# Kernel optimization log

Hardware: AMD Instinct MI355X
Metric: run time of the kernel (lower is better)

The kernel has to match this reference:

```python
import jax, jax.numpy as jnp
import numpy as np

M = 4
L_LIST = [5, 7, 9, 11]
C = 256
GC = C // M  # group channels = 64
BN_EPS = 1e-5


def setup_inputs() -> dict:
    key = jax.random.key(0)
    ks = jax.random.split(key, 12)
    B, H, W = 4, 128, 128
    x = jax.random.normal(ks[0], (B, C, H, W), dtype=jnp.float32)
    # per-group 1x1 conv weights (no bias), stacked since same shape
    qw = jax.random.normal(ks[1], (M, GC, GC), dtype=jnp.float32) * 0.05
    kw = jax.random.normal(ks[2], (M, GC, GC), dtype=jnp.float32) * 0.05
    r_q = jax.random.normal(ks[3], (1, C, 1, 1), dtype=jnp.float32)
    rk0 = jax.random.normal(ks[4], (1, GC, 2 * L_LIST[0] - 1, 1, 1), dtype=jnp.float32)
    rk1 = jax.random.normal(ks[5], (1, GC, 2 * L_LIST[1] - 1, 1, 1), dtype=jnp.float32)
    rk2 = jax.random.normal(ks[6], (1, GC, 2 * L_LIST[2] - 1, 1, 1), dtype=jnp.float32)
    rk3 = jax.random.normal(ks[7], (1, GC, 2 * L_LIST[3] - 1, 1, 1), dtype=jnp.float32)
    fusion_w = jax.random.normal(ks[8], (C, C), dtype=jnp.float32) * 0.05
    bn_gamma = jnp.ones((C,), dtype=jnp.float32)
    bn_beta = jnp.zeros((C,), dtype=jnp.float32)
    return {"x": x, "qw": qw, "kw": kw, "r_q": r_q, "rk0": rk0, "rk1": rk1,
            "rk2": rk2, "rk3": rk3, "fusion_w": fusion_w,
            "bn_gamma": bn_gamma, "bn_beta": bn_beta}


def _axial(k, L):
    """Gather the cross-shaped (axial) neighborhood of size 2L-1 per pixel.

    Matches F.unfold(k, (L,L), padding=pad) followed by slicing the center
    column (vertical neighbors) and center row minus the center element
    (horizontal neighbors), in the original ordering:
      [k_h (L vertical), k_w_pre (pad left), k_w_post (L-pad-1 right)].
    Returns [B, gc, 2L-1, H, W] with zero padding at borders.
    """
    pad = (L - 1) // 2
    B, gc, H, W = k.shape
    kv = jnp.pad(k, ((0, 0), (0, 0), (pad, pad), (0, 0)))
    kh = jnp.pad(k, ((0, 0), (0, 0), (0, 0), (pad, pad)))
    parts = [kv[:, :, r:r + H, :] for r in range(L)]            # vertical offsets -pad..pad
    parts += [kh[:, :, :, r:r + W] for r in range(pad)]          # horizontal -pad..-1
    parts += [kh[:, :, :, r:r + W] for r in range(pad + 1, L)]   # horizontal +1..+pad
    return jnp.stack(parts, axis=2)


def reference(x, qw, kw, r_q, rk0, rk1, rk2, rk3, fusion_w, bn_gamma, bn_beta):
    rks = [rk0, rk1, rk2, rk3]
    B, Cc, H, W = x.shape
    qx = r_q + x
    outs = []
    for i, L in enumerate(L_LIST):
        xg = x[:, i * GC:(i + 1) * GC]
        qg = qx[:, i * GC:(i + 1) * GC]
        q = jnp.einsum('oc,bchw->bohw', qw[i], qg)   # 1x1 conv, no bias
        k = jnp.einsum('oc,bchw->bohw', kw[i], xg)
        ka = _axial(k, L) + rks[i]                   # [B, gc, 2L-1, H, W]
        # energy over channels then summed over the 2L-1 axial positions
        e = jnp.einsum('bchw,bcrhw->bhw', q, ka)
        outs.append(jnp.broadcast_to(e[:, None], (B, GC, H, W)))
    att = jnp.concatenate(outs, axis=1)              # [B, C, H, W]
    att = jnp.einsum('oc,bchw->bohw', fusion_w, att)
    # BatchNorm2d in training mode: batch statistics over (B, H, W)
    mean = att.mean(axis=(0, 2, 3))
    var = att.var(axis=(0, 2, 3))
    att = (att - mean[:, None, None]) * jax.lax.rsqrt(var[:, None, None] + BN_EPS)
    att = att * bn_gamma[:, None, None] + bn_beta[:, None, None]
    att = jax.nn.sigmoid(jax.nn.relu(att))
    return x * att
```

## Files before the change

kernel.cpp:

```cpp
#include <hip/hip_runtime.h>

#define Bb 4
#define Cc 256
#define GC_ 64
#define Hh 128
#define Wd 128
#define HWn 16384
#define NPIX 65536
#define EPS 1e-5f

#define T_OFF   0
#define E_OFF   16777216
#define ST_OFF  (E_OFF + NPIX*4)
#define A_OFF   (ST_OFF + 16)
#define CV_OFF  (A_OFF + 16384)
#define FW_OFF  (CV_OFF + 256)

typedef __attribute__((ext_vector_type(8))) short short8v;
typedef __attribute__((ext_vector_type(4))) float f32x4;
typedef unsigned short u16;

__device__ inline u16 f2bf(float f) {
    union { float f; unsigned u; } v; v.f = f;
    unsigned r = v.u + 0x7fff + ((v.u >> 16) & 1);
    return (u16)(r >> 16);
}
__device__ inline float bf2f(u16 u) {
    union { unsigned u; float f; } v; v.u = ((unsigned)u) << 16;
    return v.f;
}

__global__ __launch_bounds__(256) void k0_precompute(
    const float* __restrict__ qw, const float* __restrict__ kw,
    const float* __restrict__ rk0, const float* __restrict__ rk1,
    const float* __restrict__ rk2, const float* __restrict__ rk3,
    const float* __restrict__ fusion_w,
    u16* __restrict__ Abf, float* __restrict__ cvec, float* __restrict__ fwred,
    float* __restrict__ stats)
{
    const int tid = threadIdx.x;
    if (blockIdx.x == 4) {
        if (tid < 16) stats[tid] = 0.f;
        for (int i = 0; i < 4; ++i) {
            float s = 0.f;
            const float* fp = fusion_w + tid*256 + i*64;
            #pragma unroll 8
            for (int c = 0; c < 64; ++c) s += fp[c];
            fwred[tid*4 + i] = s;
        }
        return;
    }
    const int g = blockIdx.x;
    __shared__ float qwL[4096];
    __shared__ float kwL[4096];
    __shared__ float rks[64];
    for (int i = tid; i < 4096; i += 256) {
        qwL[i] = qw[g*4096 + i];
        kwL[i] = kw[g*4096 + i];
    }
    __syncthreads();
    if (tid < 64) {
        const float* rkp = (g==0)?rk0:(g==1)?rk1:(g==2)?rk2:rk3;
        const int R = 4*g + 9;
        float s = 0.f;
        for (int r = 0; r < R; ++r) s += rkp[tid*R + r];
        rks[tid] = s;
    }
    __syncthreads();
    for (int idx = tid; idx < 4096; idx += 256) {
        const int ct = idx >> 10, kh = (idx >> 9) & 1;
        const int lane = (idx >> 3) & 63, j = idx & 7;
        const int c = ct*16 + (lane & 15);
        const int d = kh*32 + (lane >> 4)*8 + j;
        float s = 0.f;
        #pragma unroll
        for (int o = 0; o < 64; ++o) s += qwL[o*64 + c] * kwL[o*64 + d];
        Abf[g*4096 + idx] = f2bf(s);
    }
    if (tid < 64) {
        float s = 0.f;
        #pragma unroll
        for (int o = 0; o < 64; ++o) s += qwL[o*64 + tid] * rks[o];
        cvec[g*64 + tid] = s;
    }
}

__global__ __launch_bounds__(256) void k1_mfma(
    const float* __restrict__ x, const u16* __restrict__ Abf,
    u16* __restrict__ t, u16* __restrict__ xbf)
{
    __shared__ u16 xt[64*132];
    const int tid = threadIdx.x;
    const int wv = tid >> 6, lane = tid & 63;
    const int chunk = blockIdx.x & 127;
    const int g = (blockIdx.x >> 7) & 3;
    const int b = blockIdx.x >> 9;
    const int l15 = lane & 15, lg = lane >> 4;
    const int px0 = chunk*128;

    const u16* Ab = Abf + g*4096;
    short8v afr[4][2];
    #pragma unroll
    for (int ct = 0; ct < 4; ++ct)
      #pragma unroll
      for (int kh = 0; kh < 2; ++kh)
        afr[ct][kh] = *(const short8v*)(Ab + ((ct*2 + kh)*64 + lane)*8);

    const float* xg = x   + (size_t)(b*Cc + g*GC_)*HWn;
    u16* tg        = t    + (size_t)(b*Cc + g*GC_)*HWn;
    u16* xbg       = xbf  + (size_t)(b*Cc + g*GC_)*HWn;

    #pragma unroll
    for (int i = 0; i < 8; ++i) {
        const int idx = tid + i*256;
        const int ch = idx >> 5, q = (idx & 31) << 2;
        const float4 v = *(const float4*)(xg + (size_t)ch*HWn + px0 + q);
        u16 o4[4] __attribute__((aligned(8))) = {f2bf(v.x), f2bf(v.y), f2bf(v.z), f2bf(v.w)};
        *(uint2*)(xt + ch*132 + q) = *(const uint2*)o4;
        *(uint2*)(xbg + (size_t)ch*HWn + px0 + q) = *(const uint2*)o4;
    }
    __syncthreads();

    const int pw = wv*32;
    #pragma unroll
    for (int nt = 0; nt < 2; ++nt) {
        const int pt = pw + nt*16 + l15;
        short8v bfr[2];
        #pragma unroll
        for (int kh = 0; kh < 2; ++kh)
          #pragma unroll
          for (int j = 0; j < 8; ++j)
            bfr[kh][j] = (short)xt[(kh*32 + lg*8 + j)*132 + pt];
        #pragma unroll
        for (int ct = 0; ct < 4; ++ct) {
            f32x4 acc = {0.f, 0.f, 0.f, 0.f};
            acc = __builtin_amdgcn_mfma_f32_16x16x32_bf16(bfr[0], afr[ct][0], acc, 0, 0, 0);
            acc = __builtin_amdgcn_mfma_f32_16x16x32_bf16(bfr[1], afr[ct][1], acc, 0, 0, 0);
            u16 ov[4] __attribute__((aligned(8)));
            #pragma unroll
            for (int r = 0; r < 4; ++r) ov[r] = f2bf(acc[r]);
            *(uint2*)(tg + (size_t)(ct*16 + l15)*HWn + px0 + pw + nt*16 + lg*4) = *(const uint2*)ov;
        }
    }
}

#define TROW 132
__global__ __launch_bounds__(256) void k2_cross(
    const u16* __restrict__ t, u16* __restrict__ S)
{
    __shared__ u16 timg[42*TROW];
    __shared__ u16 simg[32*TROW];
    const int tid = threadIdx.x;
    const int bid = blockIdx.x;
    const int wk = (bid & 7)*512 + (bid >> 3);
    const int tile = wk & 3;
    const int bc = wk >> 2;
    const int g = (bc & 255) >> 6;
    const int p = g + 2;
    const int h0 = tile * 32;
    const int nrows = 32 + 2*p;
    const u16* tp = t + (size_t)bc*HWn;

    for (int idx = tid; idx < nrows*32; idx += 256) {
        const int r = idx >> 5, w4 = (idx & 31) << 2;
        const int hh = h0 - p + r;
        uint2 v = make_uint2(0u, 0u);
        if (hh >= 0 && hh < 128) v = *(const uint2*)(tp + (hh<<7) + w4);
        *(uint2*)(timg + r*TROW + w4) = v;
    }
    __syncthreads();

    {
        const int w = tid & 127;
        const int half = tid >> 7;
        const int rbase = half * 16;
        float run = 0.f;
        for (int j = 0; j <= 2*p; ++j) run += bf2f(timg[(rbase + j)*TROW + w]);
        #pragma unroll
        for (int i = 0; i < 16; ++i) {
            simg[(rbase + i)*TROW + w] = f2bf(run);
            if (i != 15)
                run += bf2f(timg[(rbase + i + 1 + 2*p)*TROW + w])
                     - bf2f(timg[(rbase + i)*TROW + w]);
        }
    }
    __syncthreads();

    {
        const int r8 = tid >> 3;
        const int seg = tid & 7;
        const int w0 = seg * 16;
        const u16* trow = timg + (r8 + p)*TROW;
        float run = 0.f;
        const int lo = max(w0 - p, 0), hi = min(w0 + p, 127);
        for (int ww = lo; ww <= hi; ++ww) run += bf2f(trow[ww]);
        u16 ov[16] __attribute__((aligned(16)));
        #pragma unroll
        for (int j = 0; j < 16; ++j) {
            const int w = w0 + j;
            const float sv = bf2f(simg[r8*TROW + w]);
            ov[j] = f2bf(run + sv - bf2f(trow[w]));
            run += (w + 1 + p < 128 ? bf2f(trow[w + 1 + p]) : 0.f)
                 - (w - p     >= 0  ? bf2f(trow[w - p])     : 0.f);
        }
        uint4* dst = (uint4*)(S + (size_t)bc*HWn + ((h0 + r8) << 7) + w0);
        dst[0] = ((const uint4*)ov)[0];
        dst[1] = ((const uint4*)ov)[1];
    }
}

__global__ __launch_bounds__(256) void k3_e(
    const u16* __restrict__ xbf, const u16* __restrict__ S,
    const float* __restrict__ r_q, const float* __restrict__ cvec,
    float* __restrict__ ebuf)
{
    const int tid = threadIdx.x;
    const int chunk = blockIdx.x & 63;
    const int g = (blockIdx.x >> 6) & 3;
    const int b = blockIdx.x >> 8;
    __shared__ float rqL[64], cvL[64];
    if (tid < 64) { rqL[tid] = r_q[g*64 + tid]; cvL[tid] = cvec[g*64 + tid]; }
    __syncthreads();
    const int p = chunk*256 + tid;
    const u16* xp = xbf + (size_t)(b*Cc + g*GC_)*HWn + p;
    const u16* Sp = S   + (size_t)(b*Cc + g*GC_)*HWn + p;
    float acc = 0.f;
    #pragma unroll 16
    for (int c = 0; c < 64; ++c)
        acc += (bf2f(xp[c*HWn]) + rqL[c]) * (bf2f(Sp[c*HWn]) + cvL[c]);
    ebuf[(b*4 + g)*HWn + p] = acc;
}

__global__ __launch_bounds__(256) void k3b_stats(
    const float* __restrict__ ebuf, float* __restrict__ stats)
{
    __shared__ float red[4*14];
    const int tid = threadIdx.x;
    const int q = blockIdx.x*256 + tid;
    const int b = q >> 14, p = q & (HWn - 1);
    const float* eb = ebuf + (size_t)b*4*HWn;
    const float e0 = eb[0*HWn + p], e1 = eb[1*HWn + p], e2 = eb[2*HWn + p], e3 = eb[3*HWn + p];
    float v[14];
    v[0]=e0; v[1]=e1; v[2]=e2; v[3]=e3;
    v[4]=e0*e0; v[5]=e0*e1; v[6]=e0*e2; v[7]=e0*e3;
    v[8]=e1*e1; v[9]=e1*e2; v[10]=e1*e3;
    v[11]=e2*e2; v[12]=e2*e3; v[13]=e3*e3;
    #pragma unroll
    for (int kk = 0; kk < 14; ++kk) {
        float s = v[kk];
        for (int off = 32; off > 0; off >>= 1) s += __shfl_down(s, off, 64);
        v[kk] = s;
    }
    const int lane = tid & 63, wv = tid >> 6;
    if (lane == 0) {
        #pragma unroll
        for (int kk = 0; kk < 14; ++kk) red[wv*14 + kk] = v[kk];
    }
    __syncthreads();
    if (tid < 14) atomicAdd(&stats[tid], red[tid] + red[14+tid] + red[28+tid] + red[42+tid]);
}

__global__ __launch_bounds__(256) void k5_out(
    const u16* __restrict__ xbf, const float* __restrict__ ebuf,
    const float* __restrict__ fwred, const float* __restrict__ stats,
    const float* __restrict__ gamma, const float* __restrict__ beta,
    float* __restrict__ out)
{
    const int tid = threadIdx.x;
    const int chunk = blockIdx.x & 15;
    const int oct = (blockIdx.x >> 4) & 31;
    const int b = blockIdx.x >> 9;
    __shared__ float alL[8], beL[8];
    __shared__ float4 fwL[8];
    if (tid < 8) {
        const int o = oct*8 + tid;
        const float invN = 1.f / (float)NPIX;
        const float me0 = stats[0]*invN, me1 = stats[1]*invN, me2 = stats[2]*invN, me3 = stats[3]*invN;
        const float m00 = stats[4]*invN,  m01 = stats[5]*invN,  m02 = stats[6]*invN,  m03 = stats[7]*invN;
        const float m11 = stats[8]*invN,  m12 = stats[9]*invN,  m13 = stats[10]*invN;
        const float m22 = stats[11]*invN, m23 = stats[12]*invN, m33 = stats[13]*invN;
        const float4 fw = ((const float4*)fwred)[o];
        const float Ef = fw.x*me0 + fw.y*me1 + fw.z*me2 + fw.w*me3;
        const float E2 = fw.x*fw.x*m00 + fw.y*fw.y*m11 + fw.z*fw.z*m22 + fw.w*fw.w*m33
                       + 2.f*(fw.x*fw.y*m01 + fw.x*fw.z*m02 + fw.x*fw.w*m03
                            + fw.y*fw.z*m12 + fw.y*fw.w*m13 + fw.z*fw.w*m23);
        const float a = gamma[o] * rsqrtf(E2 - Ef*Ef + EPS);
        alL[tid] = a;
        beL[tid] = beta[o] - Ef*a;
        fwL[tid] = fw;
    }
    __syncthreads();

    const int p0 = chunk*1024 + tid*4;
    const float* eb = ebuf + (size_t)b*4*HWn;
    const float4 E0 = *(const float4*)(eb + 0*HWn + p0);
    const float4 E1 = *(const float4*)(eb + 1*HWn + p0);
    const float4 E2v = *(const float4*)(eb + 2*HWn + p0);
    const float4 E3 = *(const float4*)(eb + 3*HWn + p0);

    #pragma unroll
    for (int c = 0; c < 8; ++c) {
        const int o = oct*8 + c;
        const float4 fw = fwL[c];
        const float al = alL[c], be = beL[c];
        float f[4];
        f[0] = fw.x*E0.x + fw.y*E1.x + fw.z*E2v.x + fw.w*E3.x;
        f[1] = fw.x*E0.y + fw.y*E1.y + fw.z*E2v.y + fw.w*E3.y;
        f[2] = fw.x*E0.z + fw.y*E1.z + fw.z*E2v.z + fw.w*E3.z;
        f[3] = fw.x*E0.w + fw.y*E1.w + fw.z*E2v.w + fw.w*E3.w;
        const size_t base = (size_t)(b*Cc + o)*HWn + p0;
        const uint2 xu = *(const uint2*)(xbf + base);
        float xa[4];
        xa[0] = bf2f((u16)(xu.x & 0xffff)); xa[1] = bf2f((u16)(xu.x >> 16));
        xa[2] = bf2f((u16)(xu.y & 0xffff)); xa[3] = bf2f((u16)(xu.y >> 16));
        float4 r; float* rp = &r.x;
        #pragma unroll
        for (int j = 0; j < 4; ++j) {
            float z = al*f[j] + be;
            z = fmaxf(z, 0.f);
            rp[j] = xa[j] / (1.f + __expf(-z));
        }
        *(float4*)(out + base) = r;
    }
}

extern "C" void kernel_launch(void* const* d_in, const int* in_sizes, int n_in,
                              void* d_out, int out_size, void* d_ws, size_t ws_size,
                              hipStream_t stream)
{
    const float* x   = (const float*)d_in[0];
    const float* qw  = (const float*)d_in[1];
    const float* kw  = (const float*)d_in[2];
    const float* r_q = (const float*)d_in[3];
    const float* rk0 = (const float*)d_in[4];
    const float* rk1 = (const float*)d_in[5];
    const float* rk2 = (const float*)d_in[6];
    const float* rk3 = (const float*)d_in[7];
    const float* fw  = (const float*)d_in[8];
    const float* gm  = (const float*)d_in[9];
    const float* bt  = (const float*)d_in[10];
    float* out = (float*)d_out;
    float* ws  = (float*)d_ws;

    u16*   t     = (u16*)(ws + T_OFF);
    u16*   xbf   = (u16*)ws + 16777216;
    float* ebuf  = ws + E_OFF;
    float* stats = ws + ST_OFF;
    u16*   Abf   = (u16*)(ws + A_OFF);
    float* cvec  = ws + CV_OFF;
    float* fwr   = ws + FW_OFF;
    u16*   Sbuf  = (u16*)out;

    k0_precompute<<<5,    256, 0, stream>>>(qw, kw, rk0, rk1, rk2, rk3, fw, Abf, cvec, fwr, stats);
    k1_mfma      <<<2048, 256, 0, stream>>>(x, Abf, t, xbf);
    k2_cross     <<<4096, 256, 0, stream>>>(t, Sbuf);
    k3_e         <<<1024, 256, 0, stream>>>(xbf, Sbuf, r_q, cvec, ebuf);
    k3b_stats    <<<256,  256, 0, stream>>>(ebuf, stats);
    k5_out       <<<2048, 256, 0, stream>>>(xbf, ebuf, fwr, stats, gm, bt, out);
}
```

Before: 109.9 us.

## Fuse cross-sum and energy kernels with double-buffered channel loop

Merges the axial cross-sum kernel and the per-pixel energy reduction into one kernel. Each block loops over 16 channels of a 16-row tile, prefetching the next channel's rows into registers and then into a second LDS buffer while it computes the current one, and accumulates energy in registers. This avoids writing and re-reading the intermediate S buffer in global memory. Four partial energy slices are written per group and summed in the stats kernel. The fused kernel launches only 512 blocks with a serial channel loop, which may reduce occupancy and latency hiding.

```diff
diff --git a/kernel.cpp b/kernel.cpp
--- a/kernel.cpp
+++ b/kernel.cpp
@@ -144,102 +144,122 @@
     }
 }
 
-#define TROW 132
-__global__ __launch_bounds__(256) void k2_cross(
-    const u16* __restrict__ t, u16* __restrict__ S)
-{
-    __shared__ u16 timg[42*TROW];
-    __shared__ u16 simg[32*TROW];
+__global__ __launch_bounds__(256) void k23_fused(
+    const u16* __restrict__ t, const u16* __restrict__ xbf,
+    const float* __restrict__ r_q, const float* __restrict__ cvec,
+    float* __restrict__ eh)
+{
+    __shared__ u16 timg[2][26*132];
+    __shared__ u16 simg[16*132];
+    __shared__ float rqL[16], cvL[16];
     const int tid = threadIdx.x;
     const int bid = blockIdx.x;
-    const int wk = (bid & 7)*512 + (bid >> 3);
-    const int tile = wk & 3;
-    const int bc = wk >> 2;
-    const int g = (bc & 255) >> 6;
+    const int wk = (bid & 7)*64 + (bid >> 3);
+    const int quarter = wk & 3;
+    const int htile = (wk >> 2) & 7;
+    const int g = (wk >> 5) & 3;
+    const int b = wk >> 7;
     const int p = g + 2;
-    const int h0 = tile * 32;
-    const int nrows = 32 + 2*p;
-    const u16* tp = t + (size_t)bc*HWn;
+    const int h0 = htile*16;
+    const int nrows = 16 + 2*p;
+    const int c0 = quarter*16;
+
+    if (tid < 16) { rqL[tid] = r_q[g*64 + c0 + tid]; cvL[tid] = cvec[g*64 + c0 + tid]; }
+
+    const u16* tbase = t   + (size_t)(b*Cc + g*GC_ + c0)*HWn;
+    const u16* xbase = xbf + (size_t)(b*Cc + g*GC_ + c0)*HWn;
 
     for (int idx = tid; idx < nrows*32; idx += 256) {
         const int r = idx >> 5, w4 = (idx & 31) << 2;
         const int hh = h0 - p + r;
         uint2 v = make_uint2(0u, 0u);
-        if (hh >= 0 && hh < 128) v = *(const uint2*)(tp + (hh<<7) + w4);
-        *(uint2*)(timg + r*TROW + w4) = v;
-    }
-    __syncthreads();
-
-    {
-        const int w = tid & 127;
-        const int half = tid >> 7;
-        const int rbase = half * 16;
-        float run = 0.f;
-        for (int j = 0; j <= 2*p; ++j) run += bf2f(timg[(rbase + j)*TROW + w]);
-        #pragma unroll
-        for (int i = 0; i < 16; ++i) {
-            simg[(rbase + i)*TROW + w] = f2bf(run);
-            if (i != 15)
-                run += bf2f(timg[(rbase + i + 1 + 2*p)*TROW + w])
-                     - bf2f(timg[(rbase + i)*TROW + w]);
-        }
-    }
-    __syncthreads();
-
-    {
-        const int r8 = tid >> 3;
-        const int seg = tid & 7;
-        const int w0 = seg * 16;
-        const u16* trow = timg + (r8 + p)*TROW;
-        float run = 0.f;
-        const int lo = max(w0 - p, 0), hi = min(w0 + p, 127);
-        for (int ww = lo; ww <= hi; ++ww) run += bf2f(trow[ww]);
-        u16 ov[16] __attribute__((aligned(16)));
-        #pragma unroll
-        for (int j = 0; j < 16; ++j) {
-            const int w = w0 + j;
-            const float sv = bf2f(simg[r8*TROW + w]);
-            ov[j] = f2bf(run + sv - bf2f(trow[w]));
-            run += (w + 1 + p < 128 ? bf2f(trow[w + 1 + p]) : 0.f)
-                 - (w - p     >= 0  ? bf2f(trow[w - p])     : 0.f);
-        }
-        uint4* dst = (uint4*)(S + (size_t)bc*HWn + ((h0 + r8) << 7) + w0);
-        dst[0] = ((const uint4*)ov)[0];
-        dst[1] = ((const uint4*)ov)[1];
-    }
-}
-
-__global__ __launch_bounds__(256) void k3_e(
-    const u16* __restrict__ xbf, const u16* __restrict__ S,
-    const float* __restrict__ r_q, const float* __restrict__ cvec,
-    float* __restrict__ ebuf)
-{
-    const int tid = threadIdx.x;
-    const int chunk = blockIdx.x & 63;
-    const int g = (blockIdx.x >> 6) & 3;
-    const int b = blockIdx.x >> 8;
-    __shared__ float rqL[64], cvL[64];
-    if (tid < 64) { rqL[tid] = r_q[g*64 + tid]; cvL[tid] = cvec[g*64 + tid]; }
-    __syncthreads();
-    const int p = chunk*256 + tid;
-    const u16* xp = xbf + (size_t)(b*Cc + g*GC_)*HWn + p;
-    const u16* Sp = S   + (size_t)(b*Cc + g*GC_)*HWn + p;
-    float acc = 0.f;
-    #pragma unroll 16
-    for (int c = 0; c < 64; ++c)
-        acc += (bf2f(xp[c*HWn]) + rqL[c]) * (bf2f(Sp[c*HWn]) + cvL[c]);
-    ebuf[(b*4 + g)*HWn + p] = acc;
+        if (hh >= 0 && hh < 128) v = *(const uint2*)(tbase + (hh<<7) + w4);
+        *(uint2*)(&timg[0][r*132 + w4]) = v;
+    }
+    __syncthreads();
+
+    const int wv_ = tid & 127, half = tid >> 7, rbase = half*8;
+    const int hr = tid >> 4, seg = tid & 15, w0 = seg*8;
+    float er[8] = {0.f,0.f,0.f,0.f,0.f,0.f,0.f,0.f};
+
+    for (int cc = 0; cc < 16; ++cc) {
+        const int cur = cc & 1;
+        uint2 pr[4]; int npr = 0;
+        if (cc < 15) {
+            const u16* tn = tbase + (size_t)(cc+1)*HWn;
+            for (int idx = tid; idx < nrows*32; idx += 256) {
+                const int r = idx >> 5, w4 = (idx & 31) << 2;
+                const int hh = h0 - p + r;
+                uint2 v = make_uint2(0u, 0u);
+                if (hh >= 0 && hh < 128) v = *(const uint2*)(tn + (hh<<7) + w4);
+                pr[npr++] = v;
+            }
+        }
+        const u16* tb = &timg[cur][0];
+
+        {
+            float run = 0.f;
+            for (int j = 0; j <= 2*p; ++j) run += bf2f(tb[(rbase + j)*132 + wv_]);
+            #pragma unroll
+            for (int i = 0; i < 8; ++i) {
+                simg[(rbase + i)*132 + wv_] = f2bf(run);
+                if (i != 7)
+                    run += bf2f(tb[(rbase + i + 1 + 2*p)*132 + wv_])
+                         - bf2f(tb[(rbase + i)*132 + wv_]);
+            }
+        }
+        __syncthreads();
+
+        {
+            const u16* trow = tb + (hr + p)*132;
+            float run = 0.f;
+            const int lo = max(w0 - p, 0), hi = min(w0 + p, 127);
+            for (int ww = lo; ww <= hi; ++ww) run += bf2f(trow[ww]);
+            const float rq = rqL[cc], cv = cvL[cc];
+            const uint4 xu = *(const uint4*)(xbase + (size_t)cc*HWn + ((h0 + hr) << 7) + w0);
+            const u16* xp = (const u16*)&xu;
+            #pragma unroll
+            for (int j = 0; j < 8; ++j) {
+                const int w = w0 + j;
+                const float S = run + bf2f(simg[hr*132 + w]) - bf2f(trow[w]);
+                er[j] += (bf2f(xp[j]) + rq) * (S + cv);
+                run += (w + 1 + p < 128 ? bf2f(trow[w + 1 + p]) : 0.f)
+                     - (w - p     >= 0  ? bf2f(trow[w - p])     : 0.f);
+            }
+        }
+        if (cc < 15) {
+            npr = 0;
+            for (int idx = tid; idx < nrows*32; idx += 256) {
+                const int r = idx >> 5, w4 = (idx & 31) << 2;
+                *(uint2*)(&timg[cur^1][r*132 + w4]) = pr[npr++];
+            }
+        }
+        __syncthreads();
+    }
+
+    float* ep = eh + (size_t)(quarter*16 + b*4 + g)*HWn + ((h0 + hr) << 7) + w0;
+    *(float4*)ep       = make_float4(er[0], er[1], er[2], er[3]);
+    *(float4*)(ep + 4) = make_float4(er[4], er[5], er[6], er[7]);
 }
 
 __global__ __launch_bounds__(256) void k3b_stats(
-    const float* __restrict__ ebuf, float* __restrict__ stats)
+    const float* __restrict__ eh, float* __restrict__ ebuf, float* __restrict__ stats)
 {
     __shared__ float red[4*14];
     const int tid = threadIdx.x;
     const int q = blockIdx.x*256 + tid;
     const int b = q >> 14, p = q & (HWn - 1);
-    const float* eb = ebuf + (size_t)b*4*HWn;
-    const float e0 = eb[0*HWn + p], e1 = eb[1*HWn + p], e2 = eb[2*HWn + p], e3 = eb[3*HWn + p];
+    float e4[4];
+    #pragma unroll
+    for (int g = 0; g < 4; ++g) {
+        float s = 0.f;
+        #pragma unroll
+        for (int qq = 0; qq < 4; ++qq)
+            s += eh[(size_t)(qq*16 + b*4 + g)*HWn + p];
+        e4[g] = s;
+        ebuf[(size_t)(b*4 + g)*HWn + p] = s;
+    }
+    const float e0 = e4[0], e1 = e4[1], e2 = e4[2], e3 = e4[3];
     float v[14];
     v[0]=e0; v[1]=e1; v[2]=e2; v[3]=e3;
     v[4]=e0*e0; v[5]=e0*e1; v[6]=e0*e2; v[7]=e0*e3;
@@ -349,12 +369,11 @@
     u16*   Abf   = (u16*)(ws + A_OFF);
     float* cvec  = ws + CV_OFF;
     float* fwr   = ws + FW_OFF;
-    u16*   Sbuf  = (u16*)out;
+    float* eh    = out;
 
     k0_precompute<<<5,    256, 0, stream>>>(qw, kw, rk0, rk1, rk2, rk3, fw, Abf, cvec, fwr, stats);
     k1_mfma      <<<2048, 256, 0, stream>>>(x, Abf, t, xbf);
-    k2_cross     <<<4096, 256, 0, stream>>>(t, Sbuf);
-    k3_e         <<<1024, 256, 0, stream>>>(xbf, Sbuf, r_q, cvec, ebuf);
-    k3b_stats    <<<256,  256, 0, stream>>>(ebuf, stats);
+    k23_fused    <<<512,  256, 0, stream>>>(t, xbf, r_q, cvec, eh);
+    k3b_stats    <<<256,  256, 0, stream>>>(eh, ebuf, stats);
     k5_out       <<<2048, 256, 0, stream>>>(xbf, ebuf, fwr, stats, gm, bt, out);
 }
```

Measured after the change: 120.6 us. 9.7% more time.
